# Kernel tuning notes

Hardware: AMD Instinct MI355X
Metric: run time of the kernel (lower is better)

Reference implementation:

```python
import jax, jax.numpy as jnp
import numpy as np

N_EMB = 1024
DIM = 256
DEPTH = 4
BETA = 10.0


def setup_inputs() -> dict:
    key = jax.random.key(0)
    k1, k2 = jax.random.split(key)
    z = jax.random.normal(k1, (32, DIM, 32, 32), dtype=jnp.float32)
    emb_w = jax.random.uniform(k2, (N_EMB, DIM), dtype=jnp.float32,
                               minval=-1.0 / N_EMB, maxval=1.0 / N_EMB)
    return {"z": z, "emb_w": emb_w}


def _quantize(zf, emb):
    # zf: [N, D], emb: [K, D]
    d = (jnp.sum(zf * zf, axis=1, keepdims=True)
         + jnp.sum(emb * emb, axis=1)
         - 2.0 * zf @ emb.T)  # [N, K]
    code = jnp.argmin(d, axis=1)  # [N]
    return emb[code], code


def reference(z, emb_w):
    B, C, H, W = z.shape
    zf = jnp.transpose(z, (0, 2, 3, 1)).reshape(-1, C)  # [N, D]
    res = jax.lax.stop_gradient(zf)  # residual_feature = z.detach()
    agg = jnp.zeros_like(zf)
    quants, codes = [], []
    for _ in range(DEPTH):
        q, code = _quantize(res, emb_w)
        res = res - q
        agg = agg + q
        quants.append(agg)
        codes.append(code)
    # commitment loss over aggregated quants
    loss = jnp.float32(0.0)
    for qa in quants:
        loss = loss + (jnp.mean((jax.lax.stop_gradient(qa) - zf) ** 2)
                       + BETA * jnp.mean((qa - jax.lax.stop_gradient(zf)) ** 2))
    codes_out = jnp.stack(codes, axis=-1).reshape(B, H, W, DEPTH)
    # straight-through: z_q = z + sg(agg - z)
    zq_f = zf + jax.lax.stop_gradient(quants[-1] - zf)
    z_q = jnp.transpose(zq_f.reshape(B, H, W, C), (0, 3, 1, 2))
    return z_q, loss, codes_out
```

## Files before the change

### kernel.cpp

```cpp
#include <hip/hip_runtime.h>


#define GLD_G const __attribute__((address_space(1))) void*
#define GLD_L __attribute__((address_space(3))) void*

__global__ __launch_bounds__(256) void prep_transpose(const float* __restrict__ emb,
                                                      float* __restrict__ embT) {
  __shared__ float tile[64][65];
  int tb = blockIdx.x;
  int c0 = (tb & 15) << 6;
  int d0 = (tb >> 4) << 6;
  int tx = threadIdx.x & 63;
  int ty = threadIdx.x >> 6;
#pragma unroll
  for (int i = 0; i < 16; ++i) {
    int c = (i << 2) + ty;
    tile[c][tx] = emb[(c0 + c) * 256 + d0 + tx];
  }
  __syncthreads();
#pragma unroll
  for (int i = 0; i < 16; ++i) {
    int d = (i << 2) + ty;
    embT[(d0 + d) * 1024 + c0 + tx] = tile[tx][d];
  }
}

__global__ __launch_bounds__(256) void prep_t2(const float* __restrict__ emb,
                                               float* __restrict__ t2,
                                               float* __restrict__ out) {
#pragma clang fp contract(off)
  __shared__ float partials[16][16];
  int ci = threadIdx.x >> 4, part = threadIdx.x & 15;
  int bb = part >> 3, jj = part & 7;
  int c = (blockIdx.x << 4) + ci;
  const float* e = emb + c * 256 + bb * 128 + jj;
  float x = e[0];
  float acc = x * x;
  for (int i = 1; i < 16; ++i) { float y = e[i * 8]; acc = acc + y * y; }
  partials[ci][part] = acc;
  __syncthreads();
  if (part == 0) {
    const float* p = partials[ci];
    float B0 = ((p[0] + p[1]) + (p[2] + p[3])) + ((p[4] + p[5]) + (p[6] + p[7]));
    float B1 = ((p[8] + p[9]) + (p[10] + p[11])) + ((p[12] + p[13]) + (p[14] + p[15]));
    t2[c] = B0 + B1;
    if (c == 0) out[8388608] = 0.0f;
  }
}

#define FM(C, A, S)                                                       \
  C.x = __builtin_fmaf(A.x, (S), C.x); C.y = __builtin_fmaf(A.y, (S), C.y); \
  C.z = __builtin_fmaf(A.z, (S), C.z); C.w = __builtin_fmaf(A.w, (S), C.w);

#define ARGMIN_ROW4(r, A0, A1, A2, A3) {                                  \
    float t1r = t1s[r];                                                   \
    float d0 = (t1r + tc.x) - 2.0f * (A0);                                \
    float d1 = (t1r + tc.y) - 2.0f * (A1);                                \
    float d2 = (t1r + tc.z) - 2.0f * (A2);                                \
    float d3 = (t1r + tc.w) - 2.0f * (A3);                                \
    float v = d0; int ci = colbase;                                       \
    if (d1 < v) { v = d1; ci = colbase + 1; }                             \
    if (d2 < v) { v = d2; ci = colbase + 2; }                             \
    if (d3 < v) { v = d3; ci = colbase + 3; }                             \
    _Pragma("unroll")                                                     \
    for (int m = 1; m < 64; m <<= 1) {                                    \
      float ov = __shfl_xor(v, m, 64);                                    \
      int oi = __shfl_xor(ci, m, 64);                                     \
      bool better = (ov < v) || (ov == v && oi < ci);                     \
      v = better ? ov : v;                                                \
      ci = better ? oi : ci;                                              \
    }                                                                     \
    if (l == 0) { redv[((r) << 2) + wg] = v; redi[((r) << 2) + wg] = ci; } }

#define STAGE(BUF, KC) {                                                  \
    int off0 = (w << 9) + (l << 2);                                       \
    __builtin_amdgcn_global_load_lds((GLD_G)(embT + ((KC) << 12) + off0), \
                                     (GLD_L)(&Bb[BUF][0] + off0), 16, 0, 0); \
    __builtin_amdgcn_global_load_lds((GLD_G)(embT + ((KC) << 12) + off0 + 256), \
                                     (GLD_L)(&Bb[BUF][0] + off0 + 256), 16, 0, 0); }

__global__ __launch_bounds__(512)
void rq_main(const float* __restrict__ z,
             const float* __restrict__ emb,
             const float* __restrict__ embT,
             const float* __restrict__ t2g,
             float* __restrict__ out) {
  __shared__ float At[256 * 36];
  __shared__ float Bb[2][4096];
  __shared__ float t2s[1024];
  __shared__ float t1part[32][16];
  __shared__ float t1s[32];
  __shared__ float redv[128];
  __shared__ int redi[128];
  __shared__ int codes_l[128];
  __shared__ float lossAcc;

  const int tid = threadIdx.x;
  const int w = tid >> 6, l = tid & 63;
  const int g = tid >> 8;
  const int wg = (tid >> 6) & 3;
  const int colbase = (tid & 255) << 2;
  const int n0 = blockIdx.x << 5;
  const int b = n0 >> 10, hw0 = n0 & 1023;
  const float* zbase = z + b * 262144 + hw0;

#pragma unroll
  for (int it = 0; it < 4; ++it) {
    int idx = it * 512 + tid;
    int k = idx >> 3, r4 = (idx & 7) << 2;
    *(float4*)(&At[k * 36 + r4]) = *(const float4*)(zbase + k * 1024 + r4);
  }
  {
    int i = tid << 1;
    float2 v = *(const float2*)(t2g + i);
    t2s[i] = v.x; t2s[i + 1] = v.y;
  }
  if (tid == 0) lossAcc = 0.0f;
  __syncthreads();

  const int rr_ = tid & 31, part_ = tid >> 5;
  const int kb0_ = (part_ >> 3) * 128 + (part_ & 7);

  for (int t = 0; t < 4; ++t) {
    STAGE(0, 0)

    {
#pragma clang fp contract(off)
      float x = At[kb0_ * 36 + rr_];
      float acc = x * x;
      for (int i = 1; i < 16; ++i) {
        float y = At[(kb0_ + i * 8) * 36 + rr_];
        acc = acc + y * y;
      }
      t1part[rr_][part_] = acc;
    }
    __syncthreads();
    if (tid < 32) {
#pragma clang fp contract(off)
      const float* p = t1part[tid];
      float B0 = ((p[0] + p[1]) + (p[2] + p[3])) + ((p[4] + p[5]) + (p[6] + p[7]));
      float B1 = ((p[8] + p[9]) + (p[10] + p[11])) + ((p[12] + p[13]) + (p[14] + p[15]));
      t1s[tid] = B0 + B1;
    }
    __syncthreads();
    if (t > 0 && tid == 0) {
      float s = 0.0f;
      for (int r = 0; r < 32; ++r) s += t1s[r];
      lossAcc += s;
    }

    float4 c00 = {0.f,0.f,0.f,0.f}, c01 = c00, c02 = c00, c03 = c00;
    float4 c10 = c00, c11 = c00, c12 = c00, c13 = c00;
    float4 c20 = c00, c21 = c00, c22 = c00, c23 = c00;
    float4 c30 = c00, c31 = c00, c32 = c00, c33 = c00;
    for (int kc = 0; kc < 64; ++kc) {
      if (kc < 63) STAGE((kc + 1) & 1, kc + 1)
      const float* bb = &Bb[kc & 1][0];
#pragma unroll
      for (int k = 0; k < 4; ++k) {
        const float* arow = &At[((kc << 2) + k) * 36 + (g << 4)];
        float4 bv = *(const float4*)(bb + (k << 10) + colbase);
        float4 a0 = *(const float4*)(arow + 0);
        float4 a1 = *(const float4*)(arow + 4);
        float4 a2 = *(const float4*)(arow + 8);
        float4 a3 = *(const float4*)(arow + 12);
        FM(c00, a0, bv.x) FM(c01, a1, bv.x) FM(c02, a2, bv.x) FM(c03, a3, bv.x)
        FM(c10, a0, bv.y) FM(c11, a1, bv.y) FM(c12, a2, bv.y) FM(c13, a3, bv.y)
        FM(c20, a0, bv.z) FM(c21, a1, bv.z) FM(c22, a2, bv.z) FM(c23, a3, bv.z)
        FM(c30, a0, bv.w) FM(c31, a1, bv.w) FM(c32, a2, bv.w) FM(c33, a3, bv.w)
      }
      __syncthreads();
    }

    {
      float4 tc = *(const float4*)(&t2s[colbase]);
      const int g16 = g << 4;
      ARGMIN_ROW4(g16 + 0,  c00.x, c10.x, c20.x, c30.x)
      ARGMIN_ROW4(g16 + 1,  c00.y, c10.y, c20.y, c30.y)
      ARGMIN_ROW4(g16 + 2,  c00.z, c10.z, c20.z, c30.z)
      ARGMIN_ROW4(g16 + 3,  c00.w, c10.w, c20.w, c30.w)
      ARGMIN_ROW4(g16 + 4,  c01.x, c11.x, c21.x, c31.x)
      ARGMIN_ROW4(g16 + 5,  c01.y, c11.y, c21.y, c31.y)
      ARGMIN_ROW4(g16 + 6,  c01.z, c11.z, c21.z, c31.z)
      ARGMIN_ROW4(g16 + 7,  c01.w, c11.w, c21.w, c31.w)
      ARGMIN_ROW4(g16 + 8,  c02.x, c12.x, c22.x, c32.x)
      ARGMIN_ROW4(g16 + 9,  c02.y, c12.y, c22.y, c32.y)
      ARGMIN_ROW4(g16 + 10, c02.z, c12.z, c22.z, c32.z)
      ARGMIN_ROW4(g16 + 11, c02.w, c12.w, c22.w, c32.w)
      ARGMIN_ROW4(g16 + 12, c03.x, c13.x, c23.x, c33.x)
      ARGMIN_ROW4(g16 + 13, c03.y, c13.y, c23.y, c33.y)
      ARGMIN_ROW4(g16 + 14, c03.z, c13.z, c23.z, c33.z)
      ARGMIN_ROW4(g16 + 15, c03.w, c13.w, c23.w, c33.w)
    }
    __syncthreads();
    if (tid < 32) {
      int r = tid;
      float v = redv[r << 2];
      int ci = redi[r << 2];
#pragma unroll
      for (int w2 = 1; w2 < 4; ++w2) {
        float ov = redv[(r << 2) + w2];
        int oi = redi[(r << 2) + w2];
        bool better = (ov < v) || (ov == v && oi < ci);
        v = better ? ov : v;
        ci = better ? oi : ci;
      }
      codes_l[(r << 2) + t] = ci;
    }
    __syncthreads();

    {
      int c = codes_l[(rr_ << 2) + t];
      const float* er = emb + (c << 8) + (part_ << 4);
      int kb = part_ << 4;
      float4 e0 = *(const float4*)(er);
      float4 e1 = *(const float4*)(er + 4);
      float4 e2 = *(const float4*)(er + 8);
      float4 e3 = *(const float4*)(er + 12);
      At[(kb + 0) * 36 + rr_] -= e0.x;  At[(kb + 1) * 36 + rr_] -= e0.y;
      At[(kb + 2) * 36 + rr_] -= e0.z;  At[(kb + 3) * 36 + rr_] -= e0.w;
      At[(kb + 4) * 36 + rr_] -= e1.x;  At[(kb + 5) * 36 + rr_] -= e1.y;
      At[(kb + 6) * 36 + rr_] -= e1.z;  At[(kb + 7) * 36 + rr_] -= e1.w;
      At[(kb + 8) * 36 + rr_] -= e2.x;  At[(kb + 9) * 36 + rr_] -= e2.y;
      At[(kb + 10) * 36 + rr_] -= e2.z; At[(kb + 11) * 36 + rr_] -= e2.w;
      At[(kb + 12) * 36 + rr_] -= e3.x; At[(kb + 13) * 36 + rr_] -= e3.y;
      At[(kb + 14) * 36 + rr_] -= e3.z; At[(kb + 15) * 36 + rr_] -= e3.w;
    }
    __syncthreads();
  }

  {
#pragma clang fp contract(off)
    float x = At[kb0_ * 36 + rr_];
    float acc = x * x;
    for (int i = 1; i < 16; ++i) {
      float y = At[(kb0_ + i * 8) * 36 + rr_];
      acc = acc + y * y;
    }
    t1part[rr_][part_] = acc;
  }
  __syncthreads();
  if (tid < 32) {
#pragma clang fp contract(off)
    const float* p = t1part[tid];
    float B0 = ((p[0] + p[1]) + (p[2] + p[3])) + ((p[4] + p[5]) + (p[6] + p[7]));
    float B1 = ((p[8] + p[9]) + (p[10] + p[11])) + ((p[12] + p[13]) + (p[14] + p[15]));
    t1s[tid] = B0 + B1;
  }
  __syncthreads();
  if (tid == 0) {
    float s = 0.0f;
    for (int r = 0; r < 32; ++r) s += t1s[r];
    float total = lossAcc + s;
    atomicAdd(out + 8388608, total * (11.0f / 8388608.0f));
  }
  __syncthreads();

  const int r0 = w << 2;
  float4 g0 = {0.f,0.f,0.f,0.f}, g1 = g0, g2 = g0, g3 = g0;
#pragma unroll
  for (int t = 0; t < 4; ++t) {
#define AGG_ROW(G, rr) {                                                  \
      int c = codes_l[((r0 + (rr)) << 2) + t];                            \
      float4 e4 = *(const float4*)(emb + (c << 8) + (l << 2));            \
      G.x += e4.x; G.y += e4.y; G.z += e4.z; G.w += e4.w; }
    AGG_ROW(g0, 0) AGG_ROW(g1, 1) AGG_ROW(g2, 2) AGG_ROW(g3, 3)
#undef AGG_ROW
  }
#define STORE_AGG(G, rr)                                                  \
  At[((l << 2) + 0) * 36 + r0 + (rr)] = G.x;                              \
  At[((l << 2) + 1) * 36 + r0 + (rr)] = G.y;                              \
  At[((l << 2) + 2) * 36 + r0 + (rr)] = G.z;                              \
  At[((l << 2) + 3) * 36 + r0 + (rr)] = G.w;
  STORE_AGG(g0, 0) STORE_AGG(g1, 1) STORE_AGG(g2, 2) STORE_AGG(g3, 3)
#undef STORE_AGG
  __syncthreads();
  float* zqbase = out + b * 262144 + hw0;
#pragma unroll
  for (int it = 0; it < 16; ++it) {
    int d = (it << 4) + (tid >> 5);
    int r = tid & 31;
    zqbase[d * 1024 + r] = At[d * 36 + r];
  }
  if (tid < 128) {
    int n = tid >> 2, tt = tid & 3;
    out[8388609 + ((n0 + n) << 2) + tt] = (float)codes_l[(n << 2) + tt];
  }
}

extern "C" void kernel_launch(void* const* d_in, const int* in_sizes, int n_in,
                              void* d_out, int out_size, void* d_ws, size_t ws_size,
                              hipStream_t stream) {
  const float* z = (const float*)d_in[0];
  const float* emb = (const float*)d_in[1];
  float* out = (float*)d_out;
  float* ws = (float*)d_ws;
  float* embT = ws;
  float* t2 = ws + 262144;

  hipLaunchKernelGGL(prep_transpose, dim3(64), dim3(256), 0, stream, emb, embT);
  hipLaunchKernelGGL(prep_t2, dim3(64), dim3(256), 0, stream, emb, t2, out);
  hipLaunchKernelGGL(rq_main, dim3(1024), dim3(512), 0, stream, z, emb, embT, t2, out);
}
```

Before: 1.118 ms.

## Read codebook directly from global memory instead of double-buffered LDS staging

Drops the async global-to-LDS double-buffered staging of the transposed codebook, along with its per-chunk barriers. Each thread now loads its float4 of codebook columns straight from global memory (L2/L1 cached) inside a single unrolled 256-step loop. The codebook-norm vector is also read from global instead of being copied into LDS. This cuts LDS footprint and synchronisation, possibly raising occupancy, but exposes the inner loop to global-load latency with no explicit prefetch.

```diff
diff --git a/kernel.cpp b/kernel.cpp
--- a/kernel.cpp
+++ b/kernel.cpp
@@ -1,8 +1,5 @@
 #include <hip/hip_runtime.h>
 
-
-#define GLD_G const __attribute__((address_space(1))) void*
-#define GLD_L __attribute__((address_space(3))) void*
 
 __global__ __launch_bounds__(256) void prep_transpose(const float* __restrict__ emb,
                                                       float* __restrict__ embT) {
@@ -72,13 +69,6 @@
     }                                                                     \
     if (l == 0) { redv[((r) << 2) + wg] = v; redi[((r) << 2) + wg] = ci; } }
 
-#define STAGE(BUF, KC) {                                                  \
-    int off0 = (w << 9) + (l << 2);                                       \
-    __builtin_amdgcn_global_load_lds((GLD_G)(embT + ((KC) << 12) + off0), \
-                                     (GLD_L)(&Bb[BUF][0] + off0), 16, 0, 0); \
-    __builtin_amdgcn_global_load_lds((GLD_G)(embT + ((KC) << 12) + off0 + 256), \
-                                     (GLD_L)(&Bb[BUF][0] + off0 + 256), 16, 0, 0); }
-
 __global__ __launch_bounds__(512)
 void rq_main(const float* __restrict__ z,
              const float* __restrict__ emb,
@@ -86,8 +76,6 @@
              const float* __restrict__ t2g,
              float* __restrict__ out) {
   __shared__ float At[256 * 36];
-  __shared__ float Bb[2][4096];
-  __shared__ float t2s[1024];
   __shared__ float t1part[32][16];
   __shared__ float t1s[32];
   __shared__ float redv[128];
@@ -110,20 +98,14 @@
     int k = idx >> 3, r4 = (idx & 7) << 2;
     *(float4*)(&At[k * 36 + r4]) = *(const float4*)(zbase + k * 1024 + r4);
   }
-  {
-    int i = tid << 1;
-    float2 v = *(const float2*)(t2g + i);
-    t2s[i] = v.x; t2s[i + 1] = v.y;
-  }
   if (tid == 0) lossAcc = 0.0f;
   __syncthreads();
 
   const int rr_ = tid & 31, part_ = tid >> 5;
   const int kb0_ = (part_ >> 3) * 128 + (part_ & 7);
+  const float* bptr = embT + colbase;
 
   for (int t = 0; t < 4; ++t) {
-    STAGE(0, 0)
-
     {
 #pragma clang fp contract(off)
       float x = At[kb0_ * 36 + rr_];
@@ -153,27 +135,22 @@
     float4 c10 = c00, c11 = c00, c12 = c00, c13 = c00;
     float4 c20 = c00, c21 = c00, c22 = c00, c23 = c00;
     float4 c30 = c00, c31 = c00, c32 = c00, c33 = c00;
-    for (int kc = 0; kc < 64; ++kc) {
-      if (kc < 63) STAGE((kc + 1) & 1, kc + 1)
-      const float* bb = &Bb[kc & 1][0];
-#pragma unroll
-      for (int k = 0; k < 4; ++k) {
-        const float* arow = &At[((kc << 2) + k) * 36 + (g << 4)];
-        float4 bv = *(const float4*)(bb + (k << 10) + colbase);
-        float4 a0 = *(const float4*)(arow + 0);
-        float4 a1 = *(const float4*)(arow + 4);
-        float4 a2 = *(const float4*)(arow + 8);
-        float4 a3 = *(const float4*)(arow + 12);
-        FM(c00, a0, bv.x) FM(c01, a1, bv.x) FM(c02, a2, bv.x) FM(c03, a3, bv.x)
-        FM(c10, a0, bv.y) FM(c11, a1, bv.y) FM(c12, a2, bv.y) FM(c13, a3, bv.y)
-        FM(c20, a0, bv.z) FM(c21, a1, bv.z) FM(c22, a2, bv.z) FM(c23, a3, bv.z)
-        FM(c30, a0, bv.w) FM(c31, a1, bv.w) FM(c32, a2, bv.w) FM(c33, a3, bv.w)
-      }
-      __syncthreads();
+#pragma unroll 4
+    for (int k = 0; k < 256; ++k) {
+      float4 bv = *(const float4*)(bptr + (k << 10));
+      const float* arow = &At[k * 36 + (g << 4)];
+      float4 a0 = *(const float4*)(arow + 0);
+      float4 a1 = *(const float4*)(arow + 4);
+      float4 a2 = *(const float4*)(arow + 8);
+      float4 a3 = *(const float4*)(arow + 12);
+      FM(c00, a0, bv.x) FM(c01, a1, bv.x) FM(c02, a2, bv.x) FM(c03, a3, bv.x)
+      FM(c10, a0, bv.y) FM(c11, a1, bv.y) FM(c12, a2, bv.y) FM(c13, a3, bv.y)
+      FM(c20, a0, bv.z) FM(c21, a1, bv.z) FM(c22, a2, bv.z) FM(c23, a3, bv.z)
+      FM(c30, a0, bv.w) FM(c31, a1, bv.w) FM(c32, a2, bv.w) FM(c33, a3, bv.w)
     }
 
     {
-      float4 tc = *(const float4*)(&t2s[colbase]);
+      float4 tc = *(const float4*)(t2g + colbase);
       const int g16 = g << 4;
       ARGMIN_ROW4(g16 + 0,  c00.x, c10.x, c20.x, c30.x)
       ARGMIN_ROW4(g16 + 1,  c00.y, c10.y, c20.y, c30.y)
```

Measured after the change: 1.012 ms. -9.5%, faster.
